# Kernel optimization log

Hardware: AMD Instinct MI355X
Metric: run time of the kernel (lower is better)

Reference implementation:

```python
import jax, jax.numpy as jnp
import numpy as np

B, S, D, H = 64, 2048, 512, 512


def setup_inputs() -> dict:
    key = jax.random.key(0)
    ks = jax.random.split(key, 8)
    scale_in = 1.0 / np.sqrt(D)
    scale_v = 1.0 / np.sqrt(H)
    return {
        "x": jax.random.normal(ks[0], (B, D), jnp.float32),
        "context": jax.random.normal(ks[1], (B, S, D), jnp.float32),
        "mask": jax.random.randint(ks[2], (B, S), 0, 2).astype(bool),
        "W_in": jax.random.normal(ks[3], (H, D), jnp.float32) * scale_in,
        "b_in": jax.random.normal(ks[4], (H,), jnp.float32) * scale_in,
        "W_ctx": jax.random.normal(ks[5], (H, D), jnp.float32) * scale_in,
        "b_ctx": jax.random.normal(ks[6], (H,), jnp.float32) * scale_in,
        "V": jax.random.uniform(ks[7], (H,), jnp.float32, -scale_v, scale_v),
    }


def reference(x, context, mask, W_in, b_in, W_ctx, b_ctx, V):
    # inp: Linear(input) -> [B, H], broadcast over S
    inp = x @ W_in.T + b_in  # [B, H]
    # ctx: 1x1 Conv1d over permuted context == per-position linear -> [B, H, S]
    ctx = jnp.einsum("bsd,hd->bhs", context, W_ctx) + b_ctx[None, :, None]
    # additive (Bahdanau) scores: V . tanh(inp + ctx) -> [B, S]
    att = jnp.einsum("h,bhs->bs", V, jnp.tanh(inp[:, :, None] + ctx))
    # mask selected positions with -inf, softmax over seq dim
    att = jnp.where(mask, -jnp.inf, att)
    alpha = jax.nn.softmax(att, axis=1)  # [B, S]
    # weighted sum of ctx columns -> [B, H]
    hidden_state = jnp.einsum("bhs,bs->bh", ctx, alpha)
    return hidden_state, alpha
```

## Files before the change

kernel.cpp:

```cpp
#include <hip/hip_runtime.h>
#include <hip/hip_bf16.h>
#include <cstdint>

#define B_ 64
#define S_ 2048
#define D_ 512
#define H_ 512

typedef short s16x8 __attribute__((ext_vector_type(8)));
typedef float f32x4 __attribute__((ext_vector_type(4)));

static __device__ __forceinline__ unsigned short f2bf(float f) {
  __bf16 h = (__bf16)f;
  return __builtin_bit_cast(unsigned short, h);
}

__global__ void k_zero(int* __restrict__ flag) {
  if (threadIdx.x == 0) *flag = 0;
}
__global__ void k_detect(const unsigned int* __restrict__ mw, int* __restrict__ flag) {
  int i = blockIdx.x * 256 + threadIdx.x;
  unsigned w = mw[i];
  int bits = 0;
  if (w == 0x3F800000u) bits = 2;
  else if (w > 1u) bits = 1;
  unsigned long long a1 = __ballot(bits & 1);
  unsigned long long a2 = __ballot(bits & 2);
  if ((threadIdx.x & 63) == 0) {
    int v = (a1 ? 1 : 0) | (a2 ? 2 : 0);
    if (v) atomicOr(flag, v);
  }
}

__global__ __launch_bounds__(256) void k_pack(const float* __restrict__ W,
                                              unsigned short* __restrict__ Wp) {
  const int tid = blockIdx.x * 256 + threadIdx.x;
  const int lane = tid & 63;
  const int hb = (tid >> 6) & 31;
  const int kb = tid >> 11;
  const int h = hb * 16 + (lane & 15);
  const int k = kb * 32 + (lane >> 4) * 8;
  const float* src = W + (size_t)h * D_ + k;
  float4 a = *(const float4*)src;
  float4 c = *(const float4*)(src + 4);
  s16x8 o;
  o[0] = (short)f2bf(a.x); o[1] = (short)f2bf(a.y);
  o[2] = (short)f2bf(a.z); o[3] = (short)f2bf(a.w);
  o[4] = (short)f2bf(c.x); o[5] = (short)f2bf(c.y);
  o[6] = (short)f2bf(c.z); o[7] = (short)f2bf(c.w);
  *(s16x8*)(Wp + (size_t)tid * 8) = o;
}

__global__ void k_inp(const float* __restrict__ x, const float* __restrict__ W_in,
                      const float* __restrict__ b_in, const float* __restrict__ b_ctx,
                      float* __restrict__ inp_pb) {
  const int b = blockIdx.x, t = threadIdx.x;
  __shared__ float xs[D_];
  xs[t] = x[b * D_ + t];
  xs[t + 256] = x[b * D_ + t + 256];
  __syncthreads();
  for (int h = t; h < H_; h += 256) {
    const float4* wr = (const float4*)(W_in + (size_t)h * D_);
    float acc = 0.f;
#pragma unroll 4
    for (int d4 = 0; d4 < 128; ++d4) {
      float4 w = wr[d4];
      acc += w.x * xs[d4 * 4] + w.y * xs[d4 * 4 + 1] + w.z * xs[d4 * 4 + 2] +
             w.w * xs[d4 * 4 + 3];
    }
    inp_pb[b * H_ + h] = acc + b_in[h] + b_ctx[h];
  }
}

__global__ __launch_bounds__(512, 2) void k_att(
    const float* __restrict__ context, const unsigned short* __restrict__ Wp,
    const float* __restrict__ inp_pb, const float* __restrict__ V,
    float* __restrict__ att) {
  __shared__ char bt[2][8192];
  __shared__ float red[8][64];
  const int tid = threadIdx.x;
  const int wave = tid >> 6, lane = tid & 63;
  const int b = blockIdx.y, s0 = blockIdx.x * 64;
  const float* ctxb = context + ((size_t)b * S_ + s0) * D_;
  const int hbase = wave * 64;
  const int bln = lane & 15, blh = lane >> 4;

  const int srow = tid >> 3, kc8 = (tid & 7) * 8;
  const int sbyte = srow * 128 + ((kc8 * 2) ^ ((srow & 7) << 4));
  const float* gsrc = ctxb + (size_t)srow * D_ + kc8;

  const unsigned short* ap = Wp + ((size_t)(wave * 4) * 64 + lane) * 8;

  f32x4 acc[4][4];
#pragma unroll
  for (int m = 0; m < 4; ++m)
#pragma unroll
    for (int n = 0; n < 4; ++n) acc[m][n] = f32x4{0.f, 0.f, 0.f, 0.f};

  f32x4 sg0a, sg0b, sg1a, sg1b, sg2a, sg2b;
#define LOAD_SET0(T) { sg0a = __builtin_nontemporal_load((const f32x4*)(gsrc + (T)*64)); \
                       sg0b = __builtin_nontemporal_load((const f32x4*)(gsrc + (T)*64 + 4)); }
#define LOAD_SET1(T) { sg1a = __builtin_nontemporal_load((const f32x4*)(gsrc + (T)*64)); \
                       sg1b = __builtin_nontemporal_load((const f32x4*)(gsrc + (T)*64 + 4)); }
#define LOAD_SET2(T) { sg2a = __builtin_nontemporal_load((const f32x4*)(gsrc + (T)*64)); \
                       sg2b = __builtin_nontemporal_load((const f32x4*)(gsrc + (T)*64 + 4)); }
#define CVT_SET(A, Bv, BUF) { s16x8 hb_; \
    hb_[0] = (short)f2bf((A)[0]); hb_[1] = (short)f2bf((A)[1]); \
    hb_[2] = (short)f2bf((A)[2]); hb_[3] = (short)f2bf((A)[3]); \
    hb_[4] = (short)f2bf((Bv)[0]); hb_[5] = (short)f2bf((Bv)[1]); \
    hb_[6] = (short)f2bf((Bv)[2]); hb_[7] = (short)f2bf((Bv)[3]); \
    *(s16x8*)(&bt[BUF][sbyte]) = hb_; }

  LOAD_SET0(0);
  LOAD_SET1(1);
  LOAD_SET2(2);
  CVT_SET(sg0a, sg0b, 0);
  asm volatile("s_waitcnt lgkmcnt(0)" ::: "memory");
  __builtin_amdgcn_s_barrier();
  __builtin_amdgcn_sched_barrier(0);

#pragma unroll
  for (int t = 0; t < 8; ++t) {
    const char* cur = bt[t & 1];
    s16x8 bfrag[2][4];
#pragma unroll
    for (int kk = 0; kk < 2; ++kk)
#pragma unroll
      for (int n = 0; n < 4; ++n) {
        const int sr = n * 16 + bln;
        const int off = (kk * 64 + blh * 16) ^ ((sr & 7) << 4);
        bfrag[kk][n] = *(const s16x8*)(cur + sr * 128 + off);
      }
    s16x8 af[2][4];
#pragma unroll
    for (int kk = 0; kk < 2; ++kk)
#pragma unroll
      for (int m = 0; m < 4; ++m)
        af[kk][m] = *(const s16x8*)(ap + (size_t)(t * 2 + kk) * 32 * 512 +
                                    (size_t)m * 512);
    if (t < 5) {
      const int s3 = (t + 3) % 3;
      if (s3 == 0) LOAD_SET0(t + 3)
      else if (s3 == 1) LOAD_SET1(t + 3)
      else LOAD_SET2(t + 3)
    }
#pragma unroll
    for (int kk = 0; kk < 2; ++kk)
#pragma unroll
      for (int m = 0; m < 4; ++m)
#pragma unroll
        for (int n = 0; n < 4; ++n)
          acc[m][n] = __builtin_amdgcn_mfma_f32_16x16x32_bf16(af[kk][m],
                                                              bfrag[kk][n],
                                                              acc[m][n], 0, 0, 0);
    if (t < 7) {
      const int s1 = (t + 1) % 3;
      const int nb = (t + 1) & 1;
      if (s1 == 0) CVT_SET(sg0a, sg0b, nb)
      else if (s1 == 1) CVT_SET(sg1a, sg1b, nb)
      else CVT_SET(sg2a, sg2b, nb)
    }
    asm volatile("s_waitcnt lgkmcnt(0)" ::: "memory");
    __builtin_amdgcn_s_barrier();
    __builtin_amdgcn_sched_barrier(0);
  }
#undef LOAD_SET0
#undef LOAD_SET1
#undef LOAD_SET2
#undef CVT_SET

  float attp[4] = {0.f, 0.f, 0.f, 0.f};
  const float* ib = inp_pb + b * H_;
#pragma unroll
  for (int m = 0; m < 4; ++m) {
#pragma unroll
    for (int j = 0; j < 4; ++j) {
      int h = hbase + m * 16 + (blh << 2) + j;
      float c = ib[h];
      float vh = V[h];
#pragma unroll
      for (int n = 0; n < 4; ++n) {
        float x = acc[m][n][j] + c;
        x = fminf(fmaxf(x, -15.f), 15.f);
        float e = __expf(2.f * x);
        attp[n] += vh * __fdividef(e - 1.f, e + 1.f);
      }
    }
  }
#pragma unroll
  for (int n = 0; n < 4; ++n) {
    attp[n] += __shfl_xor(attp[n], 16, 64);
    attp[n] += __shfl_xor(attp[n], 32, 64);
  }
  if (lane < 16) {
#pragma unroll
    for (int n = 0; n < 4; ++n) red[wave][n * 16 + lane] = attp[n];
  }
  __syncthreads();
  if (tid < 64) {
    float s = 0.f;
#pragma unroll
    for (int w = 0; w < 8; ++w) s += red[w][tid];
    att[(size_t)b * S_ + s0 + tid] = s;
  }
}

__global__ void k_softmax(const float* __restrict__ att, const void* __restrict__ mask,
                          const int* __restrict__ flag, float* __restrict__ alpha) {
  const int b = blockIdx.x, t = threadIdx.x;
  const int c = *flag;
  const int mtype = (c & 2) ? 2 : (c & 1);
  __shared__ float sm[4];
  const unsigned char* m8 = (const unsigned char*)mask;
  const int* m32 = (const int*)mask;
  const float* mf = (const float*)mask;
  float vals[8];
  float mx = -3.0e38f;
#pragma unroll
  for (int i = 0; i < 8; ++i) {
    int s = t + i * 256;
    size_t idx = (size_t)b * S_ + s;
    int msk = (mtype == 1) ? (int)m8[idx] : (mtype == 2) ? (mf[idx] != 0.f) : m32[idx];
    float v = msk ? -__builtin_inff() : att[idx];
    vals[i] = v;
    mx = fmaxf(mx, v);
  }
  for (int off = 32; off; off >>= 1) mx = fmaxf(mx, __shfl_xor(mx, off, 64));
  if ((t & 63) == 0) sm[t >> 6] = mx;
  __syncthreads();
  mx = fmaxf(fmaxf(sm[0], sm[1]), fmaxf(sm[2], sm[3]));
  float es[8];
  float sum = 0.f;
#pragma unroll
  for (int i = 0; i < 8; ++i) {
    es[i] = __expf(vals[i] - mx);
    sum += es[i];
  }
  for (int off = 32; off; off >>= 1) sum += __shfl_xor(sum, off, 64);
  __syncthreads();
  if ((t & 63) == 0) sm[t >> 6] = sum;
  __syncthreads();
  sum = sm[0] + sm[1] + sm[2] + sm[3];
  float inv = __fdividef(1.f, sum);
#pragma unroll
  for (int i = 0; i < 8; ++i) alpha[(size_t)b * S_ + t + i * 256] = es[i] * inv;
}

__global__ void k_ypart(const float* __restrict__ context,
                        const float* __restrict__ alpha, float* __restrict__ y_part) {
  const int chunk = blockIdx.x, b = blockIdx.y, t = threadIdx.x;
  __shared__ float al[256];
  __shared__ float4 part[128];
  al[t] = alpha[(size_t)b * S_ + chunk * 256 + t];
  __syncthreads();
  const int d4 = t & 127, sr = t >> 7;
  const float4* base = (const float4*)(context + ((size_t)b * S_ + chunk * 256) * D_);
  float4 acc = make_float4(0.f, 0.f, 0.f, 0.f);
  for (int i = 0; i < 128; ++i) {
    int s = sr + 2 * i;
    float4 v = base[(size_t)s * 128 + d4];
    float a = al[s];
    acc.x += a * v.x; acc.y += a * v.y; acc.z += a * v.z; acc.w += a * v.w;
  }
  if (sr == 1) part[d4] = acc;
  __syncthreads();
  if (sr == 0) {
    float4 o = part[d4];
    o.x += acc.x; o.y += acc.y; o.z += acc.z; o.w += acc.w;
    *(float4*)(y_part + ((size_t)(b * 8 + chunk)) * D_ + d4 * 4) = o;
  }
}

__global__ void k_hidden(const float* __restrict__ y_part, const float* __restrict__ W_ctx,
                         const float* __restrict__ b_ctx, float* __restrict__ hidden) {
  const int b = blockIdx.x, t = threadIdx.x;
  __shared__ float ys[D_];
  for (int d = t; d < D_; d += 256) {
    float s = 0.f;
#pragma unroll
    for (int c = 0; c < 8; ++c) s += y_part[((size_t)(b * 8 + c)) * D_ + d];
    ys[d] = s;
  }
  __syncthreads();
  for (int h = t; h < H_; h += 256) {
    const float4* wr = (const float4*)(W_ctx + (size_t)h * D_);
    float acc = 0.f;
#pragma unroll 4
    for (int d4 = 0; d4 < 128; ++d4) {
      float4 w = wr[d4];
      acc += w.x * ys[d4 * 4] + w.y * ys[d4 * 4 + 1] + w.z * ys[d4 * 4 + 2] +
             w.w * ys[d4 * 4 + 3];
    }
    hidden[b * H_ + h] = acc + b_ctx[h];
  }
}

extern "C" void kernel_launch(void* const* d_in, const int* in_sizes, int n_in,
                              void* d_out, int out_size, void* d_ws, size_t ws_size,
                              hipStream_t stream) {
  (void)in_sizes; (void)n_in; (void)out_size; (void)ws_size;
  const float* x = (const float*)d_in[0];
  const float* context = (const float*)d_in[1];
  const void* mask = d_in[2];
  const float* W_in = (const float*)d_in[3];
  const float* b_in = (const float*)d_in[4];
  const float* W_ctx = (const float*)d_in[5];
  const float* b_ctx = (const float*)d_in[6];
  const float* V = (const float*)d_in[7];

  float* out_hidden = (float*)d_out;
  float* out_alpha = (float*)d_out + B_ * H_;

  char* ws = (char*)d_ws;
  float* inp_pb = (float*)ws;
  float* att = (float*)(ws + 131072);
  float* y_part = (float*)(ws + 655360);
  int* flag = (int*)(ws + 1703936);
  unsigned short* Wp = (unsigned short*)(ws + 1704000);

  k_zero<<<1, 64, 0, stream>>>(flag);
  k_detect<<<128, 256, 0, stream>>>((const unsigned int*)mask, flag);
  k_pack<<<128, 256, 0, stream>>>(W_ctx, Wp);
  k_inp<<<B_, 256, 0, stream>>>(x, W_in, b_in, b_ctx, inp_pb);
  k_att<<<dim3(S_ / 64, B_), 512, 0, stream>>>(context, Wp, inp_pb, V, att);
  k_softmax<<<B_, 256, 0, stream>>>(att, mask, flag, out_alpha);
  k_ypart<<<dim3(8, B_), 256, 0, stream>>>(context, out_alpha, y_part);
  k_hidden<<<B_, 256, 0, stream>>>(y_part, W_ctx, b_ctx, out_hidden);
}
```

Before: 225.7 us.

## Fuse prep kernels into one launch and double-buffer A fragments in attention GEMM

Merges the zero, mask-detect, weight-pack and input-projection kernels into a single block-partitioned launch. Per-block mask flags are written instead of a global atomic, so the separate zeroing kernel is no longer needed and the softmax kernel ORs the 128 flags itself. In the attention GEMM, the W fragments for the next k-step are prefetched into a second register buffer while the current step runs, and MFMA issue priority is raised with s_setprio. This cuts launch overhead and hides global-load latency, at the cost of more registers per thread, which could reduce occupancy.

Result: slower. 233.1 us (+3.3%).

```diff
diff --git a/kernel.cpp b/kernel.cpp
--- a/kernel.cpp
+++ b/kernel.cpp
@@ -15,60 +15,63 @@
   return __builtin_bit_cast(unsigned short, h);
 }
 
-__global__ void k_zero(int* __restrict__ flag) {
-  if (threadIdx.x == 0) *flag = 0;
-}
-__global__ void k_detect(const unsigned int* __restrict__ mw, int* __restrict__ flag) {
-  int i = blockIdx.x * 256 + threadIdx.x;
-  unsigned w = mw[i];
-  int bits = 0;
-  if (w == 0x3F800000u) bits = 2;
-  else if (w > 1u) bits = 1;
-  unsigned long long a1 = __ballot(bits & 1);
-  unsigned long long a2 = __ballot(bits & 2);
-  if ((threadIdx.x & 63) == 0) {
-    int v = (a1 ? 1 : 0) | (a2 ? 2 : 0);
-    if (v) atomicOr(flag, v);
-  }
-}
-
-__global__ __launch_bounds__(256) void k_pack(const float* __restrict__ W,
-                                              unsigned short* __restrict__ Wp) {
-  const int tid = blockIdx.x * 256 + threadIdx.x;
-  const int lane = tid & 63;
-  const int hb = (tid >> 6) & 31;
-  const int kb = tid >> 11;
-  const int h = hb * 16 + (lane & 15);
-  const int k = kb * 32 + (lane >> 4) * 8;
-  const float* src = W + (size_t)h * D_ + k;
-  float4 a = *(const float4*)src;
-  float4 c = *(const float4*)(src + 4);
-  s16x8 o;
-  o[0] = (short)f2bf(a.x); o[1] = (short)f2bf(a.y);
-  o[2] = (short)f2bf(a.z); o[3] = (short)f2bf(a.w);
-  o[4] = (short)f2bf(c.x); o[5] = (short)f2bf(c.y);
-  o[6] = (short)f2bf(c.z); o[7] = (short)f2bf(c.w);
-  *(s16x8*)(Wp + (size_t)tid * 8) = o;
-}
-
-__global__ void k_inp(const float* __restrict__ x, const float* __restrict__ W_in,
-                      const float* __restrict__ b_in, const float* __restrict__ b_ctx,
-                      float* __restrict__ inp_pb) {
-  const int b = blockIdx.x, t = threadIdx.x;
-  __shared__ float xs[D_];
-  xs[t] = x[b * D_ + t];
-  xs[t + 256] = x[b * D_ + t + 256];
-  __syncthreads();
-  for (int h = t; h < H_; h += 256) {
-    const float4* wr = (const float4*)(W_in + (size_t)h * D_);
-    float acc = 0.f;
+__global__ __launch_bounds__(256) void k_prep(
+    const unsigned int* __restrict__ mw, int* __restrict__ flags,
+    const float* __restrict__ W, unsigned short* __restrict__ Wp,
+    const float* __restrict__ x, const float* __restrict__ W_in,
+    const float* __restrict__ b_in, const float* __restrict__ b_ctx,
+    float* __restrict__ inp_pb) {
+  const int bx = blockIdx.x;
+  const int t = threadIdx.x;
+  if (bx < 128) {
+    __shared__ int blk;
+    if (t == 0) blk = 0;
+    __syncthreads();
+    unsigned w = mw[bx * 256 + t];
+    int bits = 0;
+    if (w == 0x3F800000u) bits = 2;
+    else if (w > 1u) bits = 1;
+    unsigned long long a1 = __ballot(bits & 1);
+    unsigned long long a2 = __ballot(bits & 2);
+    if ((t & 63) == 0) {
+      int v = (a1 ? 1 : 0) | (a2 ? 2 : 0);
+      if (v) atomicOr(&blk, v);
+    }
+    __syncthreads();
+    if (t == 0) flags[bx] = blk;
+  } else if (bx < 256) {
+    const int tid = (bx - 128) * 256 + t;
+    const int lane = tid & 63;
+    const int hb = (tid >> 6) & 31;
+    const int kb = tid >> 11;
+    const int h = hb * 16 + (lane & 15);
+    const int k = kb * 32 + (lane >> 4) * 8;
+    const float* src = W + (size_t)h * D_ + k;
+    float4 a = *(const float4*)src;
+    float4 c = *(const float4*)(src + 4);
+    s16x8 o;
+    o[0] = (short)f2bf(a.x); o[1] = (short)f2bf(a.y);
+    o[2] = (short)f2bf(a.z); o[3] = (short)f2bf(a.w);
+    o[4] = (short)f2bf(c.x); o[5] = (short)f2bf(c.y);
+    o[6] = (short)f2bf(c.z); o[7] = (short)f2bf(c.w);
+    *(s16x8*)(Wp + (size_t)tid * 8) = o;
+  } else {
+    const int b = bx - 256;
+    __shared__ float xs[D_];
+    xs[t] = x[b * D_ + t];
+    xs[t + 256] = x[b * D_ + t + 256];
+    __syncthreads();
+    for (int h = t; h < H_; h += 256) {
+      const float4* wr = (const float4*)(W_in + (size_t)h * D_);
+      float acc = 0.f;
 #pragma unroll 4
-    for (int d4 = 0; d4 < 128; ++d4) {
-      float4 w = wr[d4];
-      acc += w.x * xs[d4 * 4] + w.y * xs[d4 * 4 + 1] + w.z * xs[d4 * 4 + 2] +
-             w.w * xs[d4 * 4 + 3];
-    }
-    inp_pb[b * H_ + h] = acc + b_in[h] + b_ctx[h];
+      for (int d4 = 0; d4 < 128; ++d4) {
+        float4 w = wr[d4];
+        acc += w.x * xs[d4 * 4] + w.y * xs[d4 * 4 + 1] + w.z * xs[d4 * 4 + 2] +
+               w.w * xs[d4 * 4 + 3];
+      }
+      inp_pb[b * H_ + h] = acc + b_in[h] + b_ctx[h];
+    }
   }
 }
 
@@ -110,10 +113,16 @@
     hb_[4] = (short)f2bf((Bv)[0]); hb_[5] = (short)f2bf((Bv)[1]); \
     hb_[6] = (short)f2bf((Bv)[2]); hb_[7] = (short)f2bf((Bv)[3]); \
     *(s16x8*)(&bt[BUF][sbyte]) = hb_; }
+#define LOAD_AF(DST, T) { _Pragma("unroll") for (int kk_ = 0; kk_ < 2; ++kk_) \
+    _Pragma("unroll") for (int m_ = 0; m_ < 4; ++m_) \
+      DST[kk_][m_] = *(const s16x8*)(ap + (size_t)((T) * 2 + kk_) * 32 * 512 + \
+                                     (size_t)m_ * 512); }
 
   LOAD_SET0(0);
   LOAD_SET1(1);
   LOAD_SET2(2);
+  s16x8 afA[2][4], afB[2][4];
+  LOAD_AF(afA, 0);
   CVT_SET(sg0a, sg0b, 0);
   asm volatile("s_waitcnt lgkmcnt(0)" ::: "memory");
   __builtin_amdgcn_s_barrier();
@@ -131,28 +140,27 @@
         const int off = (kk * 64 + blh * 16) ^ ((sr & 7) << 4);
         bfrag[kk][n] = *(const s16x8*)(cur + sr * 128 + off);
       }
-    s16x8 af[2][4];
-#pragma unroll
-    for (int kk = 0; kk < 2; ++kk)
-#pragma unroll
-      for (int m = 0; m < 4; ++m)
-        af[kk][m] = *(const s16x8*)(ap + (size_t)(t * 2 + kk) * 32 * 512 +
-                                    (size_t)m * 512);
+    if (t < 7) {
+      if ((t & 1) == 0) LOAD_AF(afB, t + 1) else LOAD_AF(afA, t + 1)
+    }
     if (t < 5) {
       const int s3 = (t + 3) % 3;
       if (s3 == 0) LOAD_SET0(t + 3)
       else if (s3 == 1) LOAD_SET1(t + 3)
       else LOAD_SET2(t + 3)
     }
+    const s16x8 (&afc)[2][4] = ((t & 1) == 0) ? afA : afB;
+    __builtin_amdgcn_s_setprio(1);
 #pragma unroll
     for (int kk = 0; kk < 2; ++kk)
 #pragma unroll
       for (int m = 0; m < 4; ++m)
 #pragma unroll
         for (int n = 0; n < 4; ++n)
-          acc[m][n] = __builtin_amdgcn_mfma_f32_16x16x32_bf16(af[kk][m],
+          acc[m][n] = __builtin_amdgcn_mfma_f32_16x16x32_bf16(afc[kk][m],
                                                               bfrag[kk][n],
                                                               acc[m][n], 0, 0, 0);
+    __builtin_amdgcn_s_setprio(0);
     if (t < 7) {
       const int s1 = (t + 1) % 3;
       const int nb = (t + 1) & 1;
@@ -168,6 +176,7 @@
 #undef LOAD_SET1
 #undef LOAD_SET2
 #undef CVT_SET
+#undef LOAD_AF
 
   float attp[4] = {0.f, 0.f, 0.f, 0.f};
   const float* ib = inp_pb + b * H_;
@@ -206,11 +215,18 @@
 }
 
 __global__ void k_softmax(const float* __restrict__ att, const void* __restrict__ mask,
-                          const int* __restrict__ flag, float* __restrict__ alpha) {
+                          const int* __restrict__ flags, float* __restrict__ alpha) {
   const int b = blockIdx.x, t = threadIdx.x;
-  const int c = *flag;
+  __shared__ int cshared;
+  __shared__ float sm[4];
+  if (t < 64) {
+    int v = flags[t] | flags[t + 64];
+    for (int off = 32; off; off >>= 1) v |= __shfl_xor(v, off, 64);
+    if (t == 0) cshared = v;
+  }
+  __syncthreads();
+  const int c = cshared;
   const int mtype = (c & 2) ? 2 : (c & 1);
-  __shared__ float sm[4];
   const unsigned char* m8 = (const unsigned char*)mask;
   const int* m32 = (const int*)mask;
   const float* mf = (const float*)mask;
@@ -315,15 +331,13 @@
   float* inp_pb = (float*)ws;
   float* att = (float*)(ws + 131072);
   float* y_part = (float*)(ws + 655360);
-  int* flag = (int*)(ws + 1703936);
-  unsigned short* Wp = (unsigned short*)(ws + 1704000);
-
-  k_zero<<<1, 64, 0, stream>>>(flag);
-  k_detect<<<128, 256, 0, stream>>>((const unsigned int*)mask, flag);
-  k_pack<<<128, 256, 0, stream>>>(W_ctx, Wp);
-  k_inp<<<B_, 256, 0, stream>>>(x, W_in, b_in, b_ctx, inp_pb);
+  int* flags = (int*)(ws + 1703936);
+  unsigned short* Wp = (unsigned short*)(ws + 1704448);
+
+  k_prep<<<320, 256, 0, stream>>>((const unsigned int*)mask, flags, W_ctx, Wp,
+                                  x, W_in, b_in, b_ctx, inp_pb);
   k_att<<<dim3(S_ / 64, B_), 512, 0, stream>>>(context, Wp, inp_pb, V, att);
-  k_softmax<<<B_, 256, 0, stream>>>(att, mask, flag, out_alpha);
+  k_softmax<<<B_, 256, 0, stream>>>(att, mask, flags, out_alpha);
   k_ypart<<<dim3(8, B_), 256, 0, stream>>>(context, out_alpha, y_part);
   k_hidden<<<B_, 256, 0, stream>>>(y_part, W_ctx, b_ctx, out_hidden);
 }
```
